# Performance work log

Hardware: AMD Instinct MI355X
Metric: run time of the kernel (lower is better)

## Reference

```python
import math
import jax, jax.numpy as jnp
import numpy as np

N_HEADS = 16
D_MODEL = 1024
USER_DIM = 512
D_K = D_MODEL // N_HEADS


def _linear_params(key, fan_in, fan_out):
    k1, k2 = jax.random.split(key)
    bound = 1.0 / math.sqrt(fan_in)
    W = jax.random.uniform(k1, (fan_in, fan_out), minval=-bound, maxval=bound, dtype=jnp.float32)
    b = jax.random.uniform(k2, (fan_out,), minval=-bound, maxval=bound, dtype=jnp.float32)
    return W, b


def setup_inputs() -> dict:
    key = jax.random.key(0)
    ks = jax.random.split(key, 7)
    B, S, Skv = 4, 2048, 2048
    query = jax.random.normal(ks[0], (B, S, D_MODEL), dtype=jnp.float32)
    k_in = jax.random.normal(ks[1], (B, Skv, USER_DIM), dtype=jnp.float32)
    v_in = jax.random.normal(ks[2], (B, Skv, USER_DIM), dtype=jnp.float32)
    Wq, bq = _linear_params(ks[3], D_MODEL, D_MODEL)
    Wk, bk = _linear_params(ks[4], USER_DIM, D_MODEL)
    Wv, bv = _linear_params(ks[5], USER_DIM, D_MODEL)
    Wo, bo = _linear_params(ks[6], D_MODEL, D_MODEL)
    return {"query": query, "key": k_in, "value": v_in,
            "Wq": Wq, "bq": bq, "Wk": Wk, "bk": bk,
            "Wv": Wv, "bv": bv, "Wo": Wo, "bo": bo}


def reference(query, key, value, Wq, bq, Wk, bk, Wv, bv, Wo, bo):
    B, S, _ = query.shape
    # zero-padding masks: rows whose raw features sum to exactly 0
    mask_key = (jnp.sum(key, axis=-1, keepdims=True) == 0)      # [B,Skv,1]
    mask_value = (jnp.sum(value, axis=-1, keepdims=True) == 0)  # [B,Skv,1]

    q = (query @ Wq + bq).reshape(B, S, N_HEADS, D_K).transpose(0, 2, 1, 3)   # [B,H,S,Dk]
    k = key @ Wk + bk
    k = jnp.where(mask_key, 0.0, k).reshape(B, -1, N_HEADS, D_K).transpose(0, 2, 1, 3)
    v = value @ Wv + bv
    v = jnp.where(mask_value, 0.0, v).reshape(B, -1, N_HEADS, D_K).transpose(0, 2, 1, 3)

    scores = jnp.einsum('bhqd,bhkd->bhqk', q, k) / math.sqrt(D_K)  # [B,H,S,Skv]
    p_attn = jax.nn.softmax(scores, axis=-1)
    # dropout is identity in eval/reference mode
    attn = jnp.einsum('bhqk,bhkd->bhqd', p_attn, v)                # [B,H,S,Dk]
    attn = attn.transpose(0, 2, 1, 3).reshape(B, S, N_HEADS * D_K)
    return attn @ Wo + bo
```

## Files before the change

kernel.cpp:

```cpp
#include <hip/hip_runtime.h>
#include <hip/hip_bf16.h>

typedef __attribute__((ext_vector_type(8))) short bf16x8;
typedef __attribute__((ext_vector_type(4))) float floatx4;
typedef __attribute__((ext_vector_type(16))) float floatx16;
typedef __attribute__((ext_vector_type(4))) unsigned short u16x4;
typedef __attribute__((ext_vector_type(4))) int intx4;

#define MFMA16(a, b, c) __builtin_amdgcn_mfma_f32_16x16x32_bf16(a, b, c, 0, 0, 0)
#define MFMA32(a, b, c) __builtin_amdgcn_mfma_f32_32x32x16_bf16(a, b, c, 0, 0, 0)

__device__ __forceinline__ unsigned short f2bf(float f) {
  unsigned int u = __float_as_uint(f);
  u += 0x7fffu + ((u >> 16) & 1u);
  return (unsigned short)(u >> 16);
}

__device__ __forceinline__ unsigned int pkbf2(float lo, float hi) {
  __hip_bfloat162 h = __float22bfloat162_rn(float2{lo, hi});
  unsigned int r;
  __builtin_memcpy(&r, &h, 4);
  return r;
}

__device__ __forceinline__ void gll16(const void* g, void* l) {
  __builtin_amdgcn_global_load_lds(
      (const __attribute__((address_space(1))) void*)g,
      (__attribute__((address_space(3))) void*)l, 16, 0, 0);
}

__global__ __launch_bounds__(256) void cvtq_kernel(const float* __restrict__ src,
                                                   unsigned short* __restrict__ dst) {
  int i = blockIdx.x * 256 + threadIdx.x;
  floatx4 v = ((const floatx4*)src)[i];
  u16x4 o;
  o[0] = f2bf(v[0]); o[1] = f2bf(v[1]); o[2] = f2bf(v[2]); o[3] = f2bf(v[3]);
  ((u16x4*)dst)[i] = o;
}

__global__ __launch_bounds__(256) void maskcvt_kernel(const float* __restrict__ src,
                                                      unsigned short* __restrict__ dst,
                                                      float* __restrict__ mask) {
  const int w = threadIdx.x >> 6, l = threadIdx.x & 63;
  const size_t row = (size_t)blockIdx.x * 4 + w;
  const float* s = src + row * 512;
  float v[8]; float sum = 0.f;
#pragma unroll
  for (int i = 0; i < 8; ++i) { v[i] = s[l + i * 64]; sum += v[i]; }
#pragma unroll
  for (int d = 1; d < 64; d <<= 1) sum += __shfl_xor(sum, d, 64);
  if (l == 0) mask[row] = (sum == 0.0f) ? 0.f : 1.f;
  unsigned short* dr = dst + row * 512;
#pragma unroll
  for (int i = 0; i < 8; ++i) dr[l + i * 64] = f2bf(v[i]);
}

__global__ __launch_bounds__(256) void wtt_kernel(const float* __restrict__ W,
                                                  unsigned short* __restrict__ Wt,
                                                  int K, float scale) {
  __shared__ float tile[32][33];
  const int tx = threadIdx.x, ty = threadIdx.y;
  const int n_ = blockIdx.x * 32 + tx;
  const int k0 = blockIdx.y * 32;
#pragma unroll
  for (int i = ty; i < 32; i += 8) tile[i][tx] = W[(size_t)(k0 + i) * 1024 + n_];
  __syncthreads();
  const int k_ = k0 + tx;
#pragma unroll
  for (int i = ty; i < 32; i += 8)
    Wt[(size_t)(blockIdx.x * 32 + i) * K + k_] = f2bf(tile[tx][i] * scale);
}

template <int MASKF, int VT, int OF32>
__global__ __launch_bounds__(256) void gemm_bt_kernel(
    const unsigned short* __restrict__ A, const unsigned short* __restrict__ Bt,
    const float* __restrict__ bias, const float* __restrict__ mask,
    void* __restrict__ outp, int M, int N, int K, float bscale) {
  __shared__ __align__(16) unsigned short As[2][128 * 32];
  __shared__ __align__(16) unsigned short Bs[2][128 * 32];
  const int t = threadIdx.x;
  const int w = t >> 6, l = t & 63, g = l >> 4, lm = l & 15;
  const int m0 = blockIdx.y * 128, n0 = blockIdx.x * 128;
  const int wm = w >> 1, wn = w & 1;
  floatx4 acc[4][4] = {};

  const int NK = K >> 5;
  auto stage = [&](int kt, int buf) {
#pragma unroll
    for (int issue = 0; issue < 2; ++issue) {
      const int tt = issue * 256 + t;
      gll16(A + (size_t)(m0 + (tt >> 2)) * K + kt * 32 + (tt & 3) * 8,
            (void*)((char*)&As[buf][0] + issue * 4096 + w * 1024));
      gll16(Bt + (size_t)(n0 + (tt >> 2)) * K + kt * 32 + (tt & 3) * 8,
            (void*)((char*)&Bs[buf][0] + issue * 4096 + w * 1024));
    }
  };

  stage(0, 0);
  int cur = 0;
  for (int kt = 0; kt < NK; ++kt) {
    __syncthreads();
    if (kt + 1 < NK) stage(kt + 1, cur ^ 1);
    const unsigned short* Ab = &As[cur][0];
    const unsigned short* Bb = &Bs[cur][0];
    bf16x8 af[4], bfr[4];
#pragma unroll
    for (int mr = 0; mr < 4; ++mr)
      af[mr] = *(const bf16x8*)(Ab + (wm * 64 + mr * 16 + lm) * 32 + g * 8);
#pragma unroll
    for (int nf = 0; nf < 4; ++nf)
      bfr[nf] = *(const bf16x8*)(Bb + (wn * 64 + nf * 16 + lm) * 32 + g * 8);
#pragma unroll
    for (int mr = 0; mr < 4; ++mr)
#pragma unroll
      for (int nf = 0; nf < 4; ++nf)
        acc[mr][nf] = MFMA16(af[mr], bfr[nf], acc[mr][nf]);
    cur ^= 1;
  }

#pragma unroll
  for (int nf = 0; nf < 4; ++nf) {
    const int n = n0 + wn * 64 + nf * 16 + lm;
    const float bv = bias[n] * bscale;
#pragma unroll
    for (int mr = 0; mr < 4; ++mr) {
      const int mb = m0 + wm * 64 + mr * 16 + g * 4;
      if (VT) {
        u16x4 pk;
#pragma unroll
        for (int j = 0; j < 4; ++j) {
          float v = acc[mr][nf][j] + bv;
          if (MASKF) v *= mask[mb + j];
          pk[j] = f2bf(v);
        }
        const int bb = mb >> 11;
        const int s = mb & 2047;
        const int sp = (s & ~12) | ((s & 8) >> 1) | ((s & 4) << 1);
        *(u16x4*)((unsigned short*)outp + ((size_t)bb * 1024 + n) * 2048 + sp) = pk;
      } else {
#pragma unroll
        for (int j = 0; j < 4; ++j) {
          float v = acc[mr][nf][j] + bv;
          if (MASKF) v *= mask[mb + j];
          if (OF32) ((float*)outp)[(size_t)(mb + j) * N + n] = v;
          else ((unsigned short*)outp)[(size_t)(mb + j) * N + n] = f2bf(v);
        }
      }
    }
  }
}

__global__ __launch_bounds__(256, 2) void flash_kernel(
    const unsigned short* __restrict__ Qp, const unsigned short* __restrict__ Kp,
    const unsigned short* __restrict__ Vt, unsigned short* __restrict__ Ctx) {
  __shared__ __align__(16) unsigned short Ks[2][64 * 64];
  __shared__ __align__(16) unsigned short Vs[2][64 * 64];
  const int t = threadIdx.x, w = t >> 6, l = t & 63, hi = l >> 5, ln = l & 31;

  const int orig = blockIdx.y * 8 + blockIdx.x;
  const int lin = (orig & 7) * 64 + (orig >> 3);
  const int bh = lin >> 3, qt = lin & 7;
  const int b = bh >> 4, h = bh & 15;
  const int q0 = qt * 256 + w * 64;
  const size_t qg = (size_t)b * 2048 + q0;

  bf16x8 qf[2][4];
#pragma unroll
  for (int s = 0; s < 2; ++s)
#pragma unroll
    for (int kc = 0; kc < 4; ++kc)
      qf[s][kc] = *(const bf16x8*)(Qp + (qg + s * 32 + ln) * 1024 + h * 64 + kc * 16 + hi * 8);

  bf16x8 onesv;
#pragma unroll
  for (int i = 0; i < 8; ++i) onesv[i] = (short)0x3F80;

  floatx16 oacc[2][2] = {};
  floatx16 smacc[2] = {};
  float mx[2] = {-3.0e38f, -3.0e38f};

  const unsigned swz2 = (unsigned)((((ln & 7) ^ ((ln >> 3) & 3)) ^ hi) << 4);

  auto stage = [&](int tile, int buf) {
#pragma unroll
    for (int issue = 0; issue < 2; ++issue) {
      const int tt = issue * 256 + t;
      const int row = tt >> 3;
      const int c = (tt & 7) ^ (row & 7) ^ ((row >> 3) & 3);
      gll16(Kp + ((size_t)b * 2048 + tile * 64 + row) * 1024 + h * 64 + c * 8,
            (void*)((char*)&Ks[buf][0] + issue * 4096 + w * 1024));
      gll16(Vt + ((size_t)b * 1024 + h * 64 + row) * 2048 + tile * 64 + c * 8,
            (void*)((char*)&Vs[buf][0] + issue * 4096 + w * 1024));
    }
  };

  stage(0, 0);
  int cur = 0;
  for (int tile = 0; tile < 32; ++tile) {
    __syncthreads();
    if (tile + 1 < 32) stage(tile + 1, cur ^ 1);

    const char* Kb = (const char*)&Ks[cur][0] + (unsigned)(ln * 128) + swz2;
    const char* Vb = (const char*)&Vs[cur][0] + (unsigned)(ln * 128) + swz2;

    bf16x8 pf[2][4];
#pragma unroll
    for (int s = 0; s < 2; ++s) {
      floatx16 sacc[2] = {};
#pragma unroll
      for (int c = 0; c < 2; ++c) {
#pragma unroll
        for (int kc = 0; kc < 4; ++kc) {
          bf16x8 kf = *(const bf16x8*)((uintptr_t)(Kb + c * 4096) ^ (unsigned)(kc * 32));
          sacc[c] = MFMA32(kf, qf[s][kc], sacc[c]);
        }
      }

      float a[8];
#pragma unroll
      for (int i = 0; i < 8; ++i) {
        const int cc = i >> 2, rr = (i & 3) * 4;
        a[i] = fmaxf(fmaxf(sacc[cc][rr], sacc[cc][rr + 1]),
                     fmaxf(sacc[cc][rr + 2], sacc[cc][rr + 3]));
      }
      float pm = fmaxf(fmaxf(fmaxf(a[0], a[1]), fmaxf(a[2], a[3])),
                       fmaxf(fmaxf(a[4], a[5]), fmaxf(a[6], a[7])));
      pm = fmaxf(pm, __shfl_xor(pm, 32, 64));
      if (!__all(pm - mx[s] <= 8.f)) {
        const float mnew = fmaxf(mx[s], pm);
        const float corr = __builtin_amdgcn_exp2f(mx[s] - mnew);
        mx[s] = mnew;
#pragma unroll
        for (int r = 0; r < 16; ++r) smacc[s][r] *= corr;
#pragma unroll
        for (int dc = 0; dc < 2; ++dc)
#pragma unroll
          for (int r = 0; r < 16; ++r) oacc[s][dc][r] *= corr;
      }
#pragma unroll
      for (int c = 0; c < 2; ++c)
#pragma unroll
        for (int r = 0; r < 16; ++r)
          sacc[c][r] = __builtin_amdgcn_exp2f(sacc[c][r] - mx[s]);

#pragma unroll
      for (int c = 0; c < 2; ++c)
#pragma unroll
        for (int h2 = 0; h2 < 2; ++h2) {
          intx4 wd;
#pragma unroll
          for (int wj = 0; wj < 4; ++wj)
            wd[wj] = (int)pkbf2(sacc[c][h2 * 8 + 2 * wj], sacc[c][h2 * 8 + 2 * wj + 1]);
          pf[s][c * 2 + h2] = __builtin_bit_cast(bf16x8, wd);
        }
    }

#pragma unroll
    for (int c = 0; c < 2; ++c)
#pragma unroll
      for (int h2 = 0; h2 < 2; ++h2) {
        const int kq = c * 2 + h2;
        smacc[0] = MFMA32(onesv, pf[0][kq], smacc[0]);
        smacc[1] = MFMA32(onesv, pf[1][kq], smacc[1]);
#pragma unroll
        for (int dc = 0; dc < 2; ++dc) {
          bf16x8 vf = *(const bf16x8*)((uintptr_t)(Vb + dc * 4096) ^ (unsigned)(c * 64 + h2 * 32));
          oacc[0][dc] = MFMA32(vf, pf[0][kq], oacc[0][dc]);
          oacc[1][dc] = MFMA32(vf, pf[1][kq], oacc[1][dc]);
        }
      }
    cur ^= 1;
  }

  __syncthreads();
  unsigned short* lds_o = &Ks[0][0] + w * 2048;
#pragma unroll
  for (int s = 0; s < 2; ++s) {
    const float inv = 1.f / smacc[s][0];
    if (s) __builtin_amdgcn_s_waitcnt(0);
#pragma unroll
    for (int dc = 0; dc < 2; ++dc)
#pragma unroll
      for (int r = 0; r < 16; r += 2) {
        const int d = dc * 32 + (r & 3) + 8 * (r >> 2) + 4 * hi;
        const unsigned int pk = pkbf2(oacc[s][dc][r] * inv, oacc[s][dc][r + 1] * inv);
        *(unsigned int*)(&lds_o[ln * 64 + (((d >> 3) ^ (ln & 7)) * 8) + (d & 7)]) = pk;
      }
    __builtin_amdgcn_s_waitcnt(0);
#pragma unroll
    for (int i = 0; i < 4; ++i) {
      const int q = i * 8 + (l >> 3);
      const int cd = l & 7;
      bf16x8 vv = *(const bf16x8*)(&lds_o[q * 64 + ((cd ^ (q & 7)) * 8)]);
      *(bf16x8*)(&Ctx[(qg + s * 32 + q) * 1024 + h * 64 + cd * 8]) = vv;
    }
  }
}

extern "C" void kernel_launch(void* const* d_in, const int* in_sizes, int n_in,
                              void* d_out, int out_size, void* d_ws, size_t ws_size,
                              hipStream_t stream) {
  const float* query = (const float*)d_in[0];
  const float* key   = (const float*)d_in[1];
  const float* value = (const float*)d_in[2];
  const float* Wq = (const float*)d_in[3];
  const float* bq = (const float*)d_in[4];
  const float* Wk = (const float*)d_in[5];
  const float* bk = (const float*)d_in[6];
  const float* Wv = (const float*)d_in[7];
  const float* bv = (const float*)d_in[8];
  const float* Wo = (const float*)d_in[9];
  const float* bo = (const float*)d_in[10];

  char* ws = (char*)d_ws;
  unsigned short* qbf = (unsigned short*)ws;  ws += (size_t)8192 * 1024 * 2;
  unsigned short* kbf = (unsigned short*)ws;  ws += (size_t)8192 * 512 * 2;
  unsigned short* vbf = (unsigned short*)ws;  ws += (size_t)8192 * 512 * 2;
  unsigned short* Wqt = (unsigned short*)ws;  ws += (size_t)1024 * 1024 * 2;
  unsigned short* Wkt = (unsigned short*)ws;  ws += (size_t)1024 * 512 * 2;
  unsigned short* Wvt = (unsigned short*)ws;  ws += (size_t)1024 * 512 * 2;
  unsigned short* Wot = (unsigned short*)ws;  ws += (size_t)1024 * 1024 * 2;
  unsigned short* Qp  = (unsigned short*)ws;  ws += (size_t)8192 * 1024 * 2;
  unsigned short* Kp  = (unsigned short*)ws;  ws += (size_t)8192 * 1024 * 2;
  unsigned short* Vtp = (unsigned short*)ws;  ws += (size_t)8192 * 1024 * 2;
  unsigned short* Ctx = (unsigned short*)ws;  ws += (size_t)8192 * 1024 * 2;
  float* maskK = (float*)ws;                  ws += (size_t)8192 * 4;
  float* maskV = (float*)ws;                  ws += (size_t)8192 * 4;

  cvtq_kernel<<<8192, 256, 0, stream>>>(query, qbf);
  maskcvt_kernel<<<2048, 256, 0, stream>>>(key, kbf, maskK);
  maskcvt_kernel<<<2048, 256, 0, stream>>>(value, vbf, maskV);
  const float QS = 0.125f * 1.44269504f;
  wtt_kernel<<<dim3(32, 32), dim3(32, 8), 0, stream>>>(Wq, Wqt, 1024, QS);
  wtt_kernel<<<dim3(32, 16), dim3(32, 8), 0, stream>>>(Wk, Wkt, 512, 1.0f);
  wtt_kernel<<<dim3(32, 16), dim3(32, 8), 0, stream>>>(Wv, Wvt, 512, 1.0f);
  wtt_kernel<<<dim3(32, 32), dim3(32, 8), 0, stream>>>(Wo, Wot, 1024, 1.0f);

  gemm_bt_kernel<0, 0, 0><<<dim3(8, 64), 256, 0, stream>>>(qbf, Wqt, bq, nullptr, Qp, 8192, 1024, 1024, QS);
  gemm_bt_kernel<1, 0, 0><<<dim3(8, 64), 256, 0, stream>>>(kbf, Wkt, bk, maskK, Kp, 8192, 1024, 512, 1.0f);
  gemm_bt_kernel<1, 1, 0><<<dim3(8, 64), 256, 0, stream>>>(vbf, Wvt, bv, maskV, Vtp, 8192, 1024, 512, 1.0f);

  flash_kernel<<<dim3(8, 64), 256, 0, stream>>>(Qp, Kp, Vtp, Ctx);

  gemm_bt_kernel<0, 0, 1><<<dim3(8, 64), 256, 0, stream>>>(Ctx, Wot, bo, nullptr, d_out, 8192, 1024, 1024, 1.0f);
}
```

Measured before the change: 238.4 us.

## Split attention KV range in two halves and merge partials in a combine kernel

The flash kernel now launches twice as many blocks, each handling half of the KV tiles. Each block writes an unnormalized bf16 partial output plus its row max and sum to workspace that reuses the bf16 input and weight buffers. A new combine kernel rescales and merges the two partials into the context tensor. The aim is more parallelism and shorter per-block loops, at the cost of extra global traffic, an additional launch, and bf16 rounding of unnormalized partial outputs.

```diff
diff --git a/kernel.cpp b/kernel.cpp
--- a/kernel.cpp
+++ b/kernel.cpp
@@ -14,6 +14,9 @@
   unsigned int u = __float_as_uint(f);
   u += 0x7fffu + ((u >> 16) & 1u);
   return (unsigned short)(u >> 16);
+}
+__device__ __forceinline__ float bf2f(unsigned short u) {
+  return __uint_as_float(((unsigned int)u) << 16);
 }
 
 __device__ __forceinline__ unsigned int pkbf2(float lo, float hi) {
@@ -152,17 +155,20 @@
 
 __global__ __launch_bounds__(256, 2) void flash_kernel(
     const unsigned short* __restrict__ Qp, const unsigned short* __restrict__ Kp,
-    const unsigned short* __restrict__ Vt, unsigned short* __restrict__ Ctx) {
+    const unsigned short* __restrict__ Vt, unsigned short* __restrict__ Opart,
+    float* __restrict__ ml) {
   __shared__ __align__(16) unsigned short Ks[2][64 * 64];
   __shared__ __align__(16) unsigned short Vs[2][64 * 64];
   const int t = threadIdx.x, w = t >> 6, l = t & 63, hi = l >> 5, ln = l & 31;
 
-  const int orig = blockIdx.y * 8 + blockIdx.x;
-  const int lin = (orig & 7) * 64 + (orig >> 3);
-  const int bh = lin >> 3, qt = lin & 7;
+  const int orig = blockIdx.y * 16 + blockIdx.x;
+  const int lin = (orig & 7) * 128 + (orig >> 3);
+  const int bh = lin >> 4, rest = lin & 15;
+  const int qt = rest >> 1, half = rest & 1;
   const int b = bh >> 4, h = bh & 15;
   const int q0 = qt * 256 + w * 64;
   const size_t qg = (size_t)b * 2048 + q0;
+  const int tbase = half * 16;
 
   bf16x8 qf[2][4];
 #pragma unroll
@@ -194,11 +200,11 @@
     }
   };
 
-  stage(0, 0);
+  stage(tbase, 0);
   int cur = 0;
-  for (int tile = 0; tile < 32; ++tile) {
+  for (int tt = 0; tt < 16; ++tt) {
     __syncthreads();
-    if (tile + 1 < 32) stage(tile + 1, cur ^ 1);
+    if (tt + 1 < 16) stage(tbase + tt + 1, cur ^ 1);
 
     const char* Kb = (const char*)&Ks[cur][0] + (unsigned)(ln * 128) + swz2;
     const char* Vb = (const char*)&Vs[cur][0] + (unsigned)(ln * 128) + swz2;
@@ -276,14 +282,17 @@
   unsigned short* lds_o = &Ks[0][0] + w * 2048;
 #pragma unroll
   for (int s = 0; s < 2; ++s) {
-    const float inv = 1.f / smacc[s][0];
+    if (hi == 0) {
+      float2 v; v.x = mx[s]; v.y = smacc[s][0];
+      ((float2*)ml)[(size_t)half * 131072 + bh * 2048 + q0 + s * 32 + ln] = v;
+    }
     if (s) __builtin_amdgcn_s_waitcnt(0);
 #pragma unroll
     for (int dc = 0; dc < 2; ++dc)
 #pragma unroll
       for (int r = 0; r < 16; r += 2) {
         const int d = dc * 32 + (r & 3) + 8 * (r >> 2) + 4 * hi;
-        const unsigned int pk = pkbf2(oacc[s][dc][r] * inv, oacc[s][dc][r + 1] * inv);
+        const unsigned int pk = pkbf2(oacc[s][dc][r], oacc[s][dc][r + 1]);
         *(unsigned int*)(&lds_o[ln * 64 + (((d >> 3) ^ (ln & 7)) * 8) + (d & 7)]) = pk;
       }
     __builtin_amdgcn_s_waitcnt(0);
@@ -292,9 +301,37 @@
       const int q = i * 8 + (l >> 3);
       const int cd = l & 7;
       bf16x8 vv = *(const bf16x8*)(&lds_o[q * 64 + ((cd ^ (q & 7)) * 8)]);
-      *(bf16x8*)(&Ctx[(qg + s * 32 + q) * 1024 + h * 64 + cd * 8]) = vv;
-    }
-  }
+      const size_t row = (size_t)bh * 2048 + q0 + s * 32 + q;
+      *(bf16x8*)(&Opart[(size_t)half * 8388608 + row * 64 + cd * 8]) = vv;
+    }
+  }
+}
+
+__global__ __launch_bounds__(256) void combine_kernel(
+    const unsigned short* __restrict__ Opart, const float* __restrict__ ml,
+    unsigned short* __restrict__ Ctx) {
+  const int r = blockIdx.x * 32 + (threadIdx.x >> 3);
+  const int d0 = (threadIdx.x & 7) * 8;
+  const float2 m1 = ((const float2*)ml)[r];
+  const float2 m2 = ((const float2*)ml)[131072 + r];
+  const float M = fmaxf(m1.x, m2.x);
+  const float w1 = __builtin_amdgcn_exp2f(m1.x - M);
+  const float w2 = __builtin_amdgcn_exp2f(m2.x - M);
+  const float L = w1 * m1.y + w2 * m2.y;
+  const float a1 = w1 / L, a2 = w2 / L;
+  const u16x4* p1 = (const u16x4*)(Opart + (size_t)r * 64 + d0);
+  const u16x4* p2 = (const u16x4*)(Opart + 8388608 + (size_t)r * 64 + d0);
+  const u16x4 o1a = p1[0], o1b = p1[1], o2a = p2[0], o2b = p2[1];
+  u16x4 ra, rb;
+#pragma unroll
+  for (int j = 0; j < 4; ++j) {
+    ra[j] = f2bf(a1 * bf2f(o1a[j]) + a2 * bf2f(o2a[j]));
+    rb[j] = f2bf(a1 * bf2f(o1b[j]) + a2 * bf2f(o2b[j]));
+  }
+  const int bh = r >> 11, q = r & 2047, b = bh >> 4, h = bh & 15;
+  unsigned short* dst = Ctx + ((size_t)b * 2048 + q) * 1024 + h * 64 + d0;
+  *(u16x4*)dst = ra;
+  *(u16x4*)(dst + 4) = rb;
 }
 
 extern "C" void kernel_launch(void* const* d_in, const int* in_sizes, int n_in,
@@ -326,6 +363,8 @@
   unsigned short* Ctx = (unsigned short*)ws;  ws += (size_t)8192 * 1024 * 2;
   float* maskK = (float*)ws;                  ws += (size_t)8192 * 4;
   float* maskV = (float*)ws;                  ws += (size_t)8192 * 4;
+  unsigned short* Opart = (unsigned short*)d_ws;
+  float* mlbuf = (float*)((char*)d_ws + 33554432);
 
   cvtq_kernel<<<8192, 256, 0, stream>>>(query, qbf);
   maskcvt_kernel<<<2048, 256, 0, stream>>>(key, kbf, maskK);
@@ -340,7 +379,8 @@
   gemm_bt_kernel<1, 0, 0><<<dim3(8, 64), 256, 0, stream>>>(kbf, Wkt, bk, maskK, Kp, 8192, 1024, 512, 1.0f);
   gemm_bt_kernel<1, 1, 0><<<dim3(8, 64), 256, 0, stream>>>(vbf, Wvt, bv, maskV, Vtp, 8192, 1024, 512, 1.0f);
 
-  flash_kernel<<<dim3(8, 64), 256, 0, stream>>>(Qp, Kp, Vtp, Ctx);
+  flash_kernel<<<dim3(16, 64), 256, 0, stream>>>(Qp, Kp, Vtp, Opart, mlbuf);
+  combine_kernel<<<4096, 256, 0, stream>>>(Opart, mlbuf, Ctx);
 
   gemm_bt_kernel<0, 0, 1><<<dim3(8, 64), 256, 0, stream>>>(Ctx, Wot, bo, nullptr, d_out, 8192, 1024, 1024, 1.0f);
 }
```

Result: slower. 248.2 us (+4.1%).
